# Performance work log

Measured on AMD Instinct MI355X. Metric: run time of the kernel, lower is better.

The kernel has to match this reference:

```python
import jax, jax.numpy as jnp
import numpy as np

N_NODES = 100000


def gcn_conv(x, W, b, src, dst, n_nodes):
    # x: [N, Fin], W: [Fin, Fout], edge (src->dst) with self-loops added,
    # symmetric normalization D^{-1/2} A D^{-1/2} as in PyG GCNConv defaults.
    h = x @ W  # [N, Fout]
    loops = jnp.arange(n_nodes, dtype=src.dtype)
    src_all = jnp.concatenate([src, loops])
    dst_all = jnp.concatenate([dst, loops])
    ones = jnp.ones(src_all.shape[0], dtype=h.dtype)
    deg = jax.ops.segment_sum(ones, dst_all, num_segments=n_nodes)  # in-degree incl. self-loop
    dinv = jnp.where(deg > 0, jax.lax.rsqrt(deg), 0.0)
    norm = dinv[src_all] * dinv[dst_all]  # [E+N]
    msg = h[src_all] * norm[:, None]      # gather + scale
    out = jax.ops.segment_sum(msg, dst_all, num_segments=n_nodes)  # scatter-add
    return out + b


def setup_inputs() -> dict:
    key = jax.random.key(0)
    k1, k2, k3, k4 = jax.random.split(key, 4)
    in_dim, hidden, out_dim = 128, 128, 64
    n_edges = 600000
    x = jax.random.normal(k1, (N_NODES, in_dim), dtype=jnp.float32)
    edge_index = jax.random.randint(k2, (2, n_edges), 0, N_NODES, dtype=jnp.int64)
    # Glorot-ish init for weights
    W1 = jax.random.normal(k3, (in_dim, hidden), dtype=jnp.float32) / np.sqrt(in_dim)
    b1 = jnp.zeros((hidden,), dtype=jnp.float32)
    W2 = jax.random.normal(k4, (hidden, out_dim), dtype=jnp.float32) / np.sqrt(hidden)
    b2 = jnp.zeros((out_dim,), dtype=jnp.float32)
    return {"x": x, "edge_index": edge_index, "W1": W1, "b1": b1, "W2": W2, "b2": b2}


def reference(x, edge_index, W1, b1, W2, b2):
    src, dst = edge_index[0], edge_index[1]
    h = jax.nn.relu(gcn_conv(x, W1, b1, src, dst, N_NODES))
    # dropout is identity in eval mode (training=False)
    return gcn_conv(h, W2, b2, src, dst, N_NODES)
```

## Files before the change

kernel.cpp:

```cpp
#include <hip/hip_runtime.h>
#include <hip/hip_bf16.h>
#include <stdint.h>

typedef unsigned int u32;
typedef unsigned short u16;
typedef unsigned long long u64;
typedef __attribute__((ext_vector_type(8))) short short8;
typedef __attribute__((ext_vector_type(4))) float f32x4;

#define SCAN_TILE 2048

__device__ __forceinline__ float bf2f(u16 u) {
    union { u32 u; float f; } v; v.u = ((u32)u) << 16; return v.f;
}
__device__ __forceinline__ u16 f2bf(float f) {
    u32 u = __float_as_uint(f);
    u32 r = (u + 0x7FFFu + ((u >> 16) & 1u)) >> 16;
    return (u16)r;
}
__device__ __forceinline__ u32 packbf(float lo, float hi) {
    return ((u32)f2bf(hi) << 16) | (u32)f2bf(lo);
}

template<int N>
__device__ __forceinline__ void wpack_one(const void* W, uint4* wpk, int p, int f32w) {
    const int n = p & (N - 1);
    const int kb = p >> ((N == 128) ? 7 : 6);
    u32 pk[4];
    if (f32w) {
        const float* wp = (const float*)W + (size_t)(kb * 8) * N + n;
        #pragma unroll
        for (int jj = 0; jj < 4; jj++)
            pk[jj] = packbf(wp[(2 * jj) * N], wp[(2 * jj + 1) * N]);
    } else {
        const u16* wp = (const u16*)W + (size_t)(kb * 8) * N + n;
        #pragma unroll
        for (int jj = 0; jj < 4; jj++)
            pk[jj] = ((u32)wp[(2 * jj + 1) * N] << 16) | (u32)wp[(2 * jj) * N];
    }
    uint4 v; v.x = pk[0]; v.y = pk[1]; v.z = pk[2]; v.w = pk[3];
    wpk[p] = v;
}

__global__ __launch_bounds__(256) void prep_k(const u32* __restrict__ xw,
                                              const u32* __restrict__ ew,
                                              int* __restrict__ flags,
                                              int* __restrict__ deg, int M,
                                              const void* __restrict__ W1,
                                              const void* __restrict__ W2,
                                              uint4* __restrict__ wpk1,
                                              uint4* __restrict__ wpk2,
                                              u64* __restrict__ lk, int nlk) {
    const int b = blockIdx.x, t = threadIdx.x;
    const int i4 = (b * 256 + t) * 4;
    if (i4 + 4 <= M) *(int4*)(deg + i4) = make_int4(0, 0, 0, 0);
    else { for (int j = 0; j < 4; j++) if (i4 + j < M) deg[i4 + j] = 0; }

    if (b < 12) {
        __shared__ int cnt;
        if (t == 0) cnt = 0;
        __syncthreads();
        int hits = 0;
        #pragma unroll
        for (int j = 0; j < 4; j++) {
            u32 f = (xw[t * 4 + j] >> 7) & 0xFFu;
            if (f >= 100u && f <= 140u) hits++;
        }
        atomicAdd(&cnt, hits);
        __syncthreads();
        const int f32w = (cnt < 512) ? 1 : 0;
        if (b < 8) wpack_one<128>(W1, wpk1, b * 256 + t, f32w);
        else       wpack_one<64> (W2, wpk2, (b - 8) * 256 + t, f32w);
        if (b == 0) {
            if (t < nlk) lk[t] = 0ull;
            if (t == 0) flags[0] = f32w;
            __shared__ u32 orr;
            if (t == 0) orr = 0u;
            __syncthreads();
            atomicOr(&orr, ew[2 * t + 1]);
            __syncthreads();
            if (t == 0) flags[1] = (orr == 0u) ? 1 : 0;
        }
    }
}

__global__ __launch_bounds__(256) void gemm1_count_k(
    const void* __restrict__ X, const uint4* __restrict__ wpk,
    u16* __restrict__ HS, const int* __restrict__ flags, int M,
    const void* __restrict__ ei, int E, int* __restrict__ deg, int GB)
{
    __shared__ u32 xlds[64 * 64];
    const int t = threadIdx.x;

    if ((int)blockIdx.x >= GB) {
        const int i2 = (((int)blockIdx.x - GB) * 256 + t) * 2;
        if (i2 >= E) return;
        if (flags[1]) {
            const long long* dp = (const long long*)ei + E;
            if (i2 + 1 < E) {
                longlong2 v = *(const longlong2*)(dp + i2);
                atomicAdd(&deg[(int)v.x], 1);
                atomicAdd(&deg[(int)v.y], 1);
            } else atomicAdd(&deg[(int)dp[i2]], 1);
        } else {
            const int* dp = (const int*)ei + E;
            if (i2 + 1 < E) {
                int2 v = *(const int2*)(dp + i2);
                atomicAdd(&deg[v.x], 1);
                atomicAdd(&deg[v.y], 1);
            } else atomicAdd(&deg[dp[i2]], 1);
        }
        return;
    }

    const int wave = t >> 6, lane = t & 63;
    const int q = lane >> 4, m = lane & 15;
    const bool xf32 = (flags[0] != 0);
    const int row0 = blockIdx.x * 64;

    for (int c = t; c < 1024; c += 256) {
        const int row = c >> 4, c8 = c & 15;
        const int grow = row0 + row;
        uint4 pk = make_uint4(0u, 0u, 0u, 0u);
        if (grow < M) {
            if (xf32) {
                const float* xp = (const float*)X + (size_t)grow * 128 + c8 * 8;
                float4 u = *(const float4*)xp;
                float4 v = *(const float4*)(xp + 4);
                pk.x = packbf(u.x, u.y); pk.y = packbf(u.z, u.w);
                pk.z = packbf(v.x, v.y); pk.w = packbf(v.z, v.w);
            } else {
                pk = *(const uint4*)((const u16*)X + (size_t)grow * 128 + c8 * 8);
            }
        }
        *(uint4*)&xlds[row * 64 + c8 * 4] = pk;
    }
    __syncthreads();

    union { uint4 u; short8 v; } a[4];
    #pragma unroll
    for (int s = 0; s < 4; s++)
        a[s].u = *(const uint4*)&xlds[(wave * 16 + m) * 64 + (s * 4 + q) * 4];

    f32x4 acc[8];
    #pragma unroll
    for (int tt = 0; tt < 8; tt++)
        acc[tt] = (f32x4){0.f, 0.f, 0.f, 0.f};

    #pragma unroll
    for (int s = 0; s < 4; s++) {
        union { uint4 u; short8 v; } b[8];
        #pragma unroll
        for (int tt = 0; tt < 8; tt++)
            b[tt].u = wpk[(s * 4 + q) * 128 + tt * 16 + m];
        #pragma unroll
        for (int tt = 0; tt < 8; tt++)
            acc[tt] = __builtin_amdgcn_mfma_f32_16x16x32_bf16(
                a[s].v, b[tt].v, acc[tt], 0, 0, 0);
    }

    u16* orow = (u16*)&xlds[wave * 16 * 64];
    #pragma unroll
    for (int tt = 0; tt < 8; tt++)
        #pragma unroll
        for (int r = 0; r < 4; r++)
            orow[(q * 4 + r) * 128 + tt * 16 + m] = f2bf(acc[tt][r]);

    #pragma unroll
    for (int j = 0; j < 4; j++) {
        const int cc = lane + j * 64;
        const int lrow = cc >> 4, c8 = cc & 15;
        const int grow = row0 + wave * 16 + lrow;
        uint4 v = *(const uint4*)&((const u32*)orow)[lrow * 64 + c8 * 4];
        if (grow < M)
            *(uint4*)(HS + (size_t)grow * 128 + c8 * 8) = v;
    }
}

__global__ __launch_bounds__(256) void scan_lb_k(const int* __restrict__ deg, int M,
                                                 u64* __restrict__ lk,
                                                 int* __restrict__ off,
                                                 int* __restrict__ cursor,
                                                 float* __restrict__ dinv, int nb) {
    const int bid = blockIdx.x, t = threadIdx.x;
    const int base = bid * SCAN_TILE + t * 8;
    int v[8];
    int s = 0;
    const bool full = (base + 8 <= M);
    if (full) {
        int4 a = *(const int4*)(deg + base);
        int4 b = *(const int4*)(deg + base + 4);
        v[0] = a.x; v[1] = a.y; v[2] = a.z; v[3] = a.w;
        v[4] = b.x; v[5] = b.y; v[6] = b.z; v[7] = b.w;
        s = v[0] + v[1] + v[2] + v[3] + v[4] + v[5] + v[6] + v[7];
    } else {
        #pragma unroll
        for (int j = 0; j < 8; j++) { v[j] = (base + j < M) ? deg[base + j] : 0; s += v[j]; }
    }
    __shared__ int buf[2][256];
    buf[0][t] = s;
    __syncthreads();
    int cur = 0;
    for (int d = 1; d < 256; d <<= 1) {
        int x = buf[cur][t];
        if (t >= d) x += buf[cur][t - d];
        buf[cur ^ 1][t] = x;
        __syncthreads();
        cur ^= 1;
    }
    const int incl = buf[cur][t];
    const int btotal = buf[cur][255];

    __shared__ int sbase;
    if (t == 0) {
        if (bid == 0) {
            __hip_atomic_store(&lk[0], (2ull << 62) | (u32)btotal,
                               __ATOMIC_RELEASE, __HIP_MEMORY_SCOPE_AGENT);
            sbase = 0;
        } else {
            __hip_atomic_store(&lk[bid], (1ull << 62) | (u32)btotal,
                               __ATOMIC_RELEASE, __HIP_MEMORY_SCOPE_AGENT);
            int run = 0;
            int j = bid - 1;
            while (j >= 0) {
                u64 w = __hip_atomic_load(&lk[j], __ATOMIC_ACQUIRE,
                                          __HIP_MEMORY_SCOPE_AGENT);
                const u64 st = w >> 62;
                if (st == 0) { __builtin_amdgcn_s_sleep(1); continue; }
                run += (int)(w & 0xFFFFFFFFull);
                if (st == 2ull) break;
                j--;
            }
            sbase = run;
            __hip_atomic_store(&lk[bid], (2ull << 62) | (u32)(run + btotal),
                               __ATOMIC_RELEASE, __HIP_MEMORY_SCOPE_AGENT);
        }
    }
    __syncthreads();

    int pre = sbase + incl - s;
    int o[8]; float dv[8];
    #pragma unroll
    for (int j = 0; j < 8; j++) {
        o[j] = pre;
        dv[j] = rsqrtf((float)(v[j] + 1));
        pre += v[j];
    }
    if (full) {
        *(int4*)(off + base)     = make_int4(o[0], o[1], o[2], o[3]);
        *(int4*)(off + base + 4) = make_int4(o[4], o[5], o[6], o[7]);
        *(int4*)(cursor + base)     = make_int4(o[0], o[1], o[2], o[3]);
        *(int4*)(cursor + base + 4) = make_int4(o[4], o[5], o[6], o[7]);
        *(float4*)(dinv + base)     = make_float4(dv[0], dv[1], dv[2], dv[3]);
        *(float4*)(dinv + base + 4) = make_float4(dv[4], dv[5], dv[6], dv[7]);
    } else {
        for (int j = 0; j < 8; j++) if (base + j < M) {
            off[base + j] = o[j]; cursor[base + j] = o[j]; dinv[base + j] = dv[j];
        }
    }
    if (bid == nb - 1 && t == 255) off[M] = sbase + btotal;
}

__global__ __launch_bounds__(256) void fill_k(const void* __restrict__ ei, int E,
                                              const int* __restrict__ flags,
                                              int* __restrict__ cursor, int* __restrict__ eidx) {
    const int i2 = (blockIdx.x * 256 + threadIdx.x) * 2;
    if (i2 >= E) return;
    int s0, d0, s1 = -1, d1 = -1;
    bool two = (i2 + 1 < E);
    if (flags[1]) {
        const long long* sp = (const long long*)ei;
        const long long* dp = sp + E;
        if (two) {
            longlong2 sv = *(const longlong2*)(sp + i2);
            longlong2 dv = *(const longlong2*)(dp + i2);
            s0 = (int)sv.x; s1 = (int)sv.y; d0 = (int)dv.x; d1 = (int)dv.y;
        } else { s0 = (int)sp[i2]; d0 = (int)dp[i2]; }
    } else {
        const int* sp = (const int*)ei;
        const int* dp = sp + E;
        if (two) {
            int2 sv = *(const int2*)(sp + i2);
            int2 dv = *(const int2*)(dp + i2);
            s0 = sv.x; s1 = sv.y; d0 = dv.x; d1 = dv.y;
        } else { s0 = sp[i2]; d0 = dp[i2]; }
    }
    int p0 = atomicAdd(&cursor[d0], 1);
    eidx[p0] = s0;
    if (two) {
        int p1 = atomicAdd(&cursor[d1], 1);
        eidx[p1] = s1;
    }
}

__global__ __launch_bounds__(256) void agg1_gemm2_k(
    const u16* __restrict__ hs, const int* __restrict__ eidx,
    const int* __restrict__ off, const float* __restrict__ dinv,
    const void* __restrict__ bias, const uint4* __restrict__ wpk,
    u16* __restrict__ HS2, const int* __restrict__ flags, int M)
{
    __shared__ u32 zlds[64 * 64];
    const int t = threadIdx.x;
    const int row0 = blockIdx.x * 64;
    const int f32io = flags[0];

    const int lane16 = t & 15;
    const int nsub   = t >> 4;
    const int c8 = lane16 * 8;
    const u16* __restrict__ hrow = hs + c8;

    float bb[8];
    if (f32io) {
        float4 u = *(const float4*)((const float*)bias + c8);
        float4 v = *(const float4*)((const float*)bias + c8 + 4);
        bb[0] = u.x; bb[1] = u.y; bb[2] = u.z; bb[3] = u.w;
        bb[4] = v.x; bb[5] = v.y; bb[6] = v.z; bb[7] = v.w;
    } else {
        uint4 u = *(const uint4*)((const u16*)bias + c8);
        const u16* s = (const u16*)&u;
        #pragma unroll
        for (int j = 0; j < 8; j++) bb[j] = bf2f(s[j]);
    }

    #pragma unroll
    for (int r = 0; r < 4; r++) {
        const int node = row0 + r * 16 + nsub;
        float o[8];
        #pragma unroll
        for (int j = 0; j < 8; j++) o[j] = 0.f;
        if (node < M) {
            const float dv = dinv[node];
            float a[8];
            {
                uint4 sp = *(const uint4*)(hrow + (size_t)node * 128);
                const u16* s = (const u16*)&sp;
                #pragma unroll
                for (int j = 0; j < 8; j++) a[j] = dv * bf2f(s[j]);
            }
            const int beg = off[node], end = off[node + 1];
            int p = beg;
            for (; p + 4 <= end; p += 4) {
                const int s0 = eidx[p + 0], s1 = eidx[p + 1];
                const int s2 = eidx[p + 2], s3 = eidx[p + 3];
                const float d0 = dinv[s0], d1 = dinv[s1];
                const float d2 = dinv[s2], d3 = dinv[s3];
                uint4 v0 = *(const uint4*)(hrow + (size_t)s0 * 128);
                uint4 v1 = *(const uint4*)(hrow + (size_t)s1 * 128);
                uint4 v2 = *(const uint4*)(hrow + (size_t)s2 * 128);
                uint4 v3 = *(const uint4*)(hrow + (size_t)s3 * 128);
                const u16* q0 = (const u16*)&v0; const u16* q1 = (const u16*)&v1;
                const u16* q2 = (const u16*)&v2; const u16* q3 = (const u16*)&v3;
                #pragma unroll
                for (int j = 0; j < 8; j++)
                    a[j] = fmaf(d0, bf2f(q0[j]),
                           fmaf(d1, bf2f(q1[j]),
                           fmaf(d2, bf2f(q2[j]),
                           fmaf(d3, bf2f(q3[j]), a[j]))));
            }
            for (; p < end; p++) {
                const int s = eidx[p];
                const float ds = dinv[s];
                uint4 v = *(const uint4*)(hrow + (size_t)s * 128);
                const u16* q = (const u16*)&v;
                #pragma unroll
                for (int j = 0; j < 8; j++) a[j] = fmaf(ds, bf2f(q[j]), a[j]);
            }
            #pragma unroll
            for (int j = 0; j < 8; j++)
                o[j] = fmaxf(fmaf(dv, a[j], bb[j]), 0.f);
        }
        uint4 pk;
        pk.x = packbf(o[0], o[1]); pk.y = packbf(o[2], o[3]);
        pk.z = packbf(o[4], o[5]); pk.w = packbf(o[6], o[7]);
        *(uint4*)&zlds[(r * 16 + nsub) * 64 + lane16 * 4] = pk;
    }
    __syncthreads();

    const int wave = t >> 6, lane = t & 63;
    const int q = lane >> 4, m = lane & 15;

    union { uint4 u; short8 v; } af[4];
    #pragma unroll
    for (int s = 0; s < 4; s++)
        af[s].u = *(const uint4*)&zlds[(wave * 16 + m) * 64 + (s * 4 + q) * 4];

    f32x4 acc[4];
    #pragma unroll
    for (int tt = 0; tt < 4; tt++)
        acc[tt] = (f32x4){0.f, 0.f, 0.f, 0.f};

    #pragma unroll
    for (int s = 0; s < 4; s++) {
        union { uint4 u; short8 v; } bf_[4];
        #pragma unroll
        for (int tt = 0; tt < 4; tt++)
            bf_[tt].u = wpk[(s * 4 + q) * 64 + tt * 16 + m];
        #pragma unroll
        for (int tt = 0; tt < 4; tt++)
            acc[tt] = __builtin_amdgcn_mfma_f32_16x16x32_bf16(
                af[s].v, bf_[tt].v, acc[tt], 0, 0, 0);
    }

    float dv4[4];
    #pragma unroll
    for (int r = 0; r < 4; r++) {
        const int grow = row0 + wave * 16 + q * 4 + r;
        dv4[r] = (grow < M) ? dinv[grow] : 0.f;
    }

    u16* orow = (u16*)&zlds[wave * 16 * 64];
    #pragma unroll
    for (int tt = 0; tt < 4; tt++)
        #pragma unroll
        for (int r = 0; r < 4; r++)
            orow[(q * 4 + r) * 64 + tt * 16 + m] = f2bf(acc[tt][r] * dv4[r]);

    #pragma unroll
    for (int j = 0; j < 2; j++) {
        const int cc = lane + j * 64;
        const int lrow = cc >> 3, c8b = cc & 7;
        const int grow = row0 + wave * 16 + lrow;
        uint4 v = *(const uint4*)&((const u32*)orow)[lrow * 32 + c8b * 4];
        if (grow < M)
            *(uint4*)(HS2 + (size_t)grow * 64 + c8b * 8) = v;
    }
}

template<int N, bool RELU>
__global__ __launch_bounds__(256) void aggregate_k(
    const u16* __restrict__ hs, const int* __restrict__ eidx,
    const int* __restrict__ off, const float* __restrict__ dinv,
    const void* __restrict__ bias, void* __restrict__ out,
    const int* __restrict__ flags, int out_is_ext, int M)
{
    constexpr int TPN = N / 8;
    constexpr int NPB = 256 / TPN;
    const int node = blockIdx.x * NPB + threadIdx.x / TPN;
    const int lane = threadIdx.x % TPN;
    if (node >= M) return;
    const int f32io = flags[0];
    const int beg = off[node], end = off[node + 1];
    const int c8 = lane * 8;
    const u16* __restrict__ hrow = hs + c8;

    float a[8];
    {
        uint4 sp = *(const uint4*)(hrow + (size_t)node * N);
        const u16* s = (const u16*)&sp;
        #pragma unroll
        for (int j = 0; j < 8; j++) a[j] = bf2f(s[j]);
    }

    int p = beg;
    for (; p + 4 <= end; p += 4) {
        const int s0 = eidx[p + 0], s1 = eidx[p + 1];
        const int s2 = eidx[p + 2], s3 = eidx[p + 3];
        uint4 v0 = *(const uint4*)(hrow + (size_t)s0 * N);
        uint4 v1 = *(const uint4*)(hrow + (size_t)s1 * N);
        uint4 v2 = *(const uint4*)(hrow + (size_t)s2 * N);
        uint4 v3 = *(const uint4*)(hrow + (size_t)s3 * N);
        const u16* q0 = (const u16*)&v0; const u16* q1 = (const u16*)&v1;
        const u16* q2 = (const u16*)&v2; const u16* q3 = (const u16*)&v3;
        #pragma unroll
        for (int j = 0; j < 8; j++)
            a[j] += (bf2f(q0[j]) + bf2f(q1[j])) + (bf2f(q2[j]) + bf2f(q3[j]));
    }
    for (; p < end; p++) {
        const int s = eidx[p];
        uint4 v = *(const uint4*)(hrow + (size_t)s * N);
        const u16* q = (const u16*)&v;
        #pragma unroll
        for (int j = 0; j < 8; j++) a[j] += bf2f(q[j]);
    }

    const float dv = dinv[node];
    float b[8];
    if (f32io) {
        float4 u = *(const float4*)((const float*)bias + c8);
        float4 v = *(const float4*)((const float*)bias + c8 + 4);
        b[0] = u.x; b[1] = u.y; b[2] = u.z; b[3] = u.w;
        b[4] = v.x; b[5] = v.y; b[6] = v.z; b[7] = v.w;
    } else {
        uint4 u = *(const uint4*)((const u16*)bias + c8);
        const u16* s = (const u16*)&u;
        #pragma unroll
        for (int j = 0; j < 8; j++) b[j] = bf2f(s[j]);
    }
    float o[8];
    #pragma unroll
    for (int j = 0; j < 8; j++) {
        o[j] = fmaf(dv, a[j], b[j]);
        if (RELU) o[j] = fmaxf(o[j], 0.f);
    }
    if (out_is_ext && f32io) {
        float* op = (float*)out + (size_t)node * N + c8;
        *(float4*)op       = make_float4(o[0], o[1], o[2], o[3]);
        *(float4*)(op + 4) = make_float4(o[4], o[5], o[6], o[7]);
    } else {
        uint4 pk;
        pk.x = packbf(o[0], o[1]); pk.y = packbf(o[2], o[3]);
        pk.z = packbf(o[4], o[5]); pk.w = packbf(o[6], o[7]);
        *(uint4*)((u16*)out + (size_t)node * N + c8) = pk;
    }
}

extern "C" void kernel_launch(void* const* d_in, const int* in_sizes, int n_in,
                              void* d_out, int out_size, void* d_ws, size_t ws_size,
                              hipStream_t stream) {
    const void* x  = d_in[0];
    const void* ei = d_in[1];
    const void* W1 = d_in[2];
    const void* b1 = d_in[3];
    const void* W2 = d_in[4];
    const void* b2 = d_in[5];

    const int M = in_sizes[0] / 128;
    const int E = in_sizes[1] / 2;
    const int NB = (M + SCAN_TILE - 1) / SCAN_TILE;
    const int GB = (M + 63) / 64;
    const int CB = (E + 511) / 512;

    char* ws = (char*)d_ws;
    size_t offb = 0;
    auto alloc = [&](size_t bytes) -> void* {
        void* p = ws + offb; offb += (bytes + 255) & ~(size_t)255; return p;
    };
    int*   flags  = (int*)  alloc(256);
    u64*   lk     = (u64*)  alloc(2048);
    uint4* wpk1   = (uint4*)alloc(16 * 128 * 16);
    uint4* wpk2   = (uint4*)alloc(16 * 64 * 16);
    int*   deg    = (int*)  alloc((size_t)M * 4);
    int*   off    = (int*)  alloc((size_t)(M + 1) * 4);
    int*   cursor = (int*)  alloc((size_t)M * 4);
    float* dinv   = (float*)alloc((size_t)M * 4);
    int*   eidx   = (int*)  alloc((size_t)E * 4);
    u16*   hs1    = (u16*)  alloc((size_t)M * 128 * 2);
    u16*   hs2    = (u16*)  alloc((size_t)M * 64 * 2);
    (void)ws_size; (void)n_in; (void)out_size;

    prep_k<<<(M + 1023) / 1024, 256, 0, stream>>>((const u32*)x, (const u32*)ei, flags,
                                                  deg, M, W1, W2, wpk1, wpk2, lk, NB);
    gemm1_count_k<<<GB + CB, 256, 0, stream>>>(x, wpk1, hs1, flags, M, ei, E, deg, GB);
    scan_lb_k<<<NB, 256, 0, stream>>>(deg, M, lk, off, cursor, dinv, NB);
    fill_k<<<(E + 511) / 512, 256, 0, stream>>>(ei, E, flags, cursor, eidx);
    agg1_gemm2_k<<<(M + 63) / 64, 256, 0, stream>>>(hs1, eidx, off, dinv, b1, wpk2, hs2,
                                                    flags, M);
    aggregate_k<64, false><<<(M + 31) / 32, 256, 0, stream>>>(hs2, eidx, off, dinv, b2, d_out,
                                                              flags, 1, M);
}
```

Before: 235.3 us.

## Restructure kernel pipeline: fuse degree count into prep, scan into gemm1, stage edges in LDS

Degree zeroing moves to a memset, and degree counting moves into the prep kernel, which detects index width per block. The scan is merged with the first GEMM into one launch. The aggregation kernels stage their CSR offsets and edge indices in LDS. The first aggregation interleaves four nodes per thread so their gathers are in flight at once, which trades extra registers and divergence for more memory-level parallelism. The goal is fewer launches and better latency hiding on the gathers.

New measurement: 230.9 us. About the same (-1.9%).

```diff
diff --git a/kernel.cpp b/kernel.cpp
--- a/kernel.cpp
+++ b/kernel.cpp
@@ -42,22 +42,20 @@
     wpk[p] = v;
 }
 
-__global__ __launch_bounds__(256) void prep_k(const u32* __restrict__ xw,
-                                              const u32* __restrict__ ew,
-                                              int* __restrict__ flags,
-                                              int* __restrict__ deg, int M,
-                                              const void* __restrict__ W1,
-                                              const void* __restrict__ W2,
-                                              uint4* __restrict__ wpk1,
-                                              uint4* __restrict__ wpk2,
-                                              u64* __restrict__ lk, int nlk) {
+__global__ __launch_bounds__(256) void prep_count_k(
+    const u32* __restrict__ xw, const void* __restrict__ ei,
+    int* __restrict__ flags, int M, int E,
+    const void* __restrict__ W1, const void* __restrict__ W2,
+    uint4* __restrict__ wpk1, uint4* __restrict__ wpk2,
+    int* __restrict__ deg)
+{
+    __shared__ int cnt;
+    __shared__ u32 orr;
+    __shared__ u32 dorr;
     const int b = blockIdx.x, t = threadIdx.x;
-    const int i4 = (b * 256 + t) * 4;
-    if (i4 + 4 <= M) *(int4*)(deg + i4) = make_int4(0, 0, 0, 0);
-    else { for (int j = 0; j < 4; j++) if (i4 + j < M) deg[i4 + j] = 0; }
+    const u32* ew = (const u32*)ei;
 
     if (b < 12) {
-        __shared__ int cnt;
         if (t == 0) cnt = 0;
         __syncthreads();
         int hits = 0;
@@ -72,51 +70,141 @@
         if (b < 8) wpack_one<128>(W1, wpk1, b * 256 + t, f32w);
         else       wpack_one<64> (W2, wpk2, (b - 8) * 256 + t, f32w);
         if (b == 0) {
-            if (t < nlk) lk[t] = 0ull;
             if (t == 0) flags[0] = f32w;
-            __shared__ u32 orr;
             if (t == 0) orr = 0u;
             __syncthreads();
             atomicOr(&orr, ew[2 * t + 1]);
             __syncthreads();
             if (t == 0) flags[1] = (orr == 0u) ? 1 : 0;
         }
-    }
-}
-
-__global__ __launch_bounds__(256) void gemm1_count_k(
+        return;
+    }
+
+    const int cb = b - 12;
+    const int i2 = (cb * 256 + t) * 2;
+    if (t == 0) dorr = 0u;
+    __syncthreads();
+    u32 w = 0u;
+    if (i2 + 1 < E) w = ew[(size_t)E + i2 + 1];
+    atomicOr(&dorr, w);
+    __syncthreads();
+    const bool is64 = (dorr == 0u);
+    if (i2 >= E) return;
+    if (is64) {
+        const long long* dp = (const long long*)ei + E;
+        if (i2 + 1 < E) {
+            longlong2 v = *(const longlong2*)(dp + i2);
+            atomicAdd(&deg[(int)v.x], 1);
+            atomicAdd(&deg[(int)v.y], 1);
+        } else atomicAdd(&deg[(int)dp[i2]], 1);
+    } else {
+        const int* dp = (const int*)ei + E;
+        if (i2 + 1 < E) {
+            int2 v = *(const int2*)(dp + i2);
+            atomicAdd(&deg[v.x], 1);
+            atomicAdd(&deg[v.y], 1);
+        } else atomicAdd(&deg[dp[i2]], 1);
+    }
+}
+
+__global__ __launch_bounds__(256) void scan_gemm1_k(
+    const int* __restrict__ deg, int M,
+    u64* __restrict__ lk, int* __restrict__ off,
+    int* __restrict__ cursor, float* __restrict__ dinv, int nb,
     const void* __restrict__ X, const uint4* __restrict__ wpk,
-    u16* __restrict__ HS, const int* __restrict__ flags, int M,
-    const void* __restrict__ ei, int E, int* __restrict__ deg, int GB)
+    u16* __restrict__ HS, const int* __restrict__ flags)
 {
-    __shared__ u32 xlds[64 * 64];
+    __shared__ u32 smem[64 * 64];
     const int t = threadIdx.x;
 
-    if ((int)blockIdx.x >= GB) {
-        const int i2 = (((int)blockIdx.x - GB) * 256 + t) * 2;
-        if (i2 >= E) return;
-        if (flags[1]) {
-            const long long* dp = (const long long*)ei + E;
-            if (i2 + 1 < E) {
-                longlong2 v = *(const longlong2*)(dp + i2);
-                atomicAdd(&deg[(int)v.x], 1);
-                atomicAdd(&deg[(int)v.y], 1);
-            } else atomicAdd(&deg[(int)dp[i2]], 1);
+    if ((int)blockIdx.x < nb) {
+        const int bid = blockIdx.x;
+        const int base = bid * SCAN_TILE + t * 8;
+        int v[8];
+        int s = 0;
+        const bool full = (base + 8 <= M);
+        if (full) {
+            int4 a = *(const int4*)(deg + base);
+            int4 b = *(const int4*)(deg + base + 4);
+            v[0] = a.x; v[1] = a.y; v[2] = a.z; v[3] = a.w;
+            v[4] = b.x; v[5] = b.y; v[6] = b.z; v[7] = b.w;
+            s = v[0] + v[1] + v[2] + v[3] + v[4] + v[5] + v[6] + v[7];
         } else {
-            const int* dp = (const int*)ei + E;
-            if (i2 + 1 < E) {
-                int2 v = *(const int2*)(dp + i2);
-                atomicAdd(&deg[v.x], 1);
-                atomicAdd(&deg[v.y], 1);
-            } else atomicAdd(&deg[dp[i2]], 1);
-        }
+            #pragma unroll
+            for (int j = 0; j < 8; j++) { v[j] = (base + j < M) ? deg[base + j] : 0; s += v[j]; }
+        }
+        int* bp = (int*)smem;
+        int* bq = (int*)smem + 256;
+        int* psb = (int*)smem + 512;
+        bp[t] = s;
+        __syncthreads();
+        for (int d = 1; d < 256; d <<= 1) {
+            int x = bp[t];
+            if (t >= d) x += bp[t - d];
+            bq[t] = x;
+            __syncthreads();
+            int* tmp = bp; bp = bq; bq = tmp;
+        }
+        const int incl = bp[t];
+        const int btotal = bp[255];
+
+        if (t == 0) {
+            if (bid == 0) {
+                __hip_atomic_store(&lk[0], (2ull << 62) | (u32)btotal,
+                                   __ATOMIC_RELEASE, __HIP_MEMORY_SCOPE_AGENT);
+                psb[0] = 0;
+            } else {
+                __hip_atomic_store(&lk[bid], (1ull << 62) | (u32)btotal,
+                                   __ATOMIC_RELEASE, __HIP_MEMORY_SCOPE_AGENT);
+                int run = 0;
+                int j = bid - 1;
+                while (j >= 0) {
+                    u64 w = __hip_atomic_load(&lk[j], __ATOMIC_ACQUIRE,
+                                              __HIP_MEMORY_SCOPE_AGENT);
+                    const u64 st = w >> 62;
+                    if (st == 0) { __builtin_amdgcn_s_sleep(1); continue; }
+                    run += (int)(w & 0xFFFFFFFFull);
+                    if (st == 2ull) break;
+                    j--;
+                }
+                psb[0] = run;
+                __hip_atomic_store(&lk[bid], (2ull << 62) | (u32)(run + btotal),
+                                   __ATOMIC_RELEASE, __HIP_MEMORY_SCOPE_AGENT);
+            }
+        }
+        __syncthreads();
+        const int sbase = psb[0];
+
+        int pre = sbase + incl - s;
+        int o[8]; float dv[8];
+        #pragma unroll
+        for (int j = 0; j < 8; j++) {
+            o[j] = pre;
+            dv[j] = rsqrtf((float)(v[j] + 1));
+            pre += v[j];
+        }
+        if (full) {
+            *(int4*)(off + base)     = make_int4(o[0], o[1], o[2], o[3]);
+            *(int4*)(off + base + 4) = make_int4(o[4], o[5], o[6], o[7]);
+            *(int4*)(cursor + base)     = make_int4(o[0], o[1], o[2], o[3]);
+            *(int4*)(cursor + base + 4) = make_int4(o[4], o[5], o[6], o[7]);
+            *(float4*)(dinv + base)     = make_float4(dv[0], dv[1], dv[2], dv[3]);
+            *(float4*)(dinv + base + 4) = make_float4(dv[4], dv[5], dv[6], dv[7]);
+        } else {
+            for (int j = 0; j < 8; j++) if (base + j < M) {
+                off[base + j] = o[j]; cursor[base + j] = o[j]; dinv[base + j] = dv[j];
+            }
+        }
+        if (bid == nb - 1 && t == 255) off[M] = sbase + btotal;
         return;
     }
 
+    const int gb = (int)blockIdx.x - nb;
     const int wave = t >> 6, lane = t & 63;
     const int q = lane >> 4, m = lane & 15;
     const bool xf32 = (flags[0] != 0);
-    const int row0 = blockIdx.x * 64;
+    const int row0 = gb * 64;
+    u32* xlds = smem;
 
     for (int c = t; c < 1024; c += 256) {
         const int row = c >> 4, c8 = c & 15;
@@ -175,90 +263,6 @@
         if (grow < M)
             *(uint4*)(HS + (size_t)grow * 128 + c8 * 8) = v;
     }
-}
-
-__global__ __launch_bounds__(256) void scan_lb_k(const int* __restrict__ deg, int M,
-                                                 u64* __restrict__ lk,
-                                                 int* __restrict__ off,
-                                                 int* __restrict__ cursor,
-                                                 float* __restrict__ dinv, int nb) {
-    const int bid = blockIdx.x, t = threadIdx.x;
-    const int base = bid * SCAN_TILE + t * 8;
-    int v[8];
-    int s = 0;
-    const bool full = (base + 8 <= M);
-    if (full) {
-        int4 a = *(const int4*)(deg + base);
-        int4 b = *(const int4*)(deg + base + 4);
-        v[0] = a.x; v[1] = a.y; v[2] = a.z; v[3] = a.w;
-        v[4] = b.x; v[5] = b.y; v[6] = b.z; v[7] = b.w;
-        s = v[0] + v[1] + v[2] + v[3] + v[4] + v[5] + v[6] + v[7];
-    } else {
-        #pragma unroll
-        for (int j = 0; j < 8; j++) { v[j] = (base + j < M) ? deg[base + j] : 0; s += v[j]; }
-    }
-    __shared__ int buf[2][256];
-    buf[0][t] = s;
-    __syncthreads();
-    int cur = 0;
-    for (int d = 1; d < 256; d <<= 1) {
-        int x = buf[cur][t];
-        if (t >= d) x += buf[cur][t - d];
-        buf[cur ^ 1][t] = x;
-        __syncthreads();
-        cur ^= 1;
-    }
-    const int incl = buf[cur][t];
-    const int btotal = buf[cur][255];
-
-    __shared__ int sbase;
-    if (t == 0) {
-        if (bid == 0) {
-            __hip_atomic_store(&lk[0], (2ull << 62) | (u32)btotal,
-                               __ATOMIC_RELEASE, __HIP_MEMORY_SCOPE_AGENT);
-            sbase = 0;
-        } else {
-            __hip_atomic_store(&lk[bid], (1ull << 62) | (u32)btotal,
-                               __ATOMIC_RELEASE, __HIP_MEMORY_SCOPE_AGENT);
-            int run = 0;
-            int j = bid - 1;
-            while (j >= 0) {
-                u64 w = __hip_atomic_load(&lk[j], __ATOMIC_ACQUIRE,
-                                          __HIP_MEMORY_SCOPE_AGENT);
-                const u64 st = w >> 62;
-                if (st == 0) { __builtin_amdgcn_s_sleep(1); continue; }
-                run += (int)(w & 0xFFFFFFFFull);
-                if (st == 2ull) break;
-                j--;
-            }
-            sbase = run;
-            __hip_atomic_store(&lk[bid], (2ull << 62) | (u32)(run + btotal),
-                               __ATOMIC_RELEASE, __HIP_MEMORY_SCOPE_AGENT);
-        }
-    }
-    __syncthreads();
-
-    int pre = sbase + incl - s;
-    int o[8]; float dv[8];
-    #pragma unroll
-    for (int j = 0; j < 8; j++) {
-        o[j] = pre;
-        dv[j] = rsqrtf((float)(v[j] + 1));
-        pre += v[j];
-    }
-    if (full) {
-        *(int4*)(off + base)     = make_int4(o[0], o[1], o[2], o[3]);
-        *(int4*)(off + base + 4) = make_int4(o[4], o[5], o[6], o[7]);
-        *(int4*)(cursor + base)     = make_int4(o[0], o[1], o[2], o[3]);
-        *(int4*)(cursor + base + 4) = make_int4(o[4], o[5], o[6], o[7]);
-        *(float4*)(dinv + base)     = make_float4(dv[0], dv[1], dv[2], dv[3]);
-        *(float4*)(dinv + base + 4) = make_float4(dv[4], dv[5], dv[6], dv[7]);
-    } else {
-        for (int j = 0; j < 8; j++) if (base + j < M) {
-            off[base + j] = o[j]; cursor[base + j] = o[j]; dinv[base + j] = dv[j];
-        }
-    }
-    if (bid == nb - 1 && t == 255) off[M] = sbase + btotal;
 }
 
 __global__ __launch_bounds__(256) void fill_k(const void* __restrict__ ei, int E,
@@ -300,12 +304,21 @@
     u16* __restrict__ HS2, const int* __restrict__ flags, int M)
 {
     __shared__ u32 zlds[64 * 64];
+    __shared__ int soff[65];
+    __shared__ int elds[768];
     const int t = threadIdx.x;
     const int row0 = blockIdx.x * 64;
     const int f32io = flags[0];
 
-    const int lane16 = t & 15;
-    const int nsub   = t >> 4;
+    for (int i = t; i <= 64; i += 256) soff[i] = off[min(row0 + i, M)];
+    __syncthreads();
+    const int beg64 = soff[0];
+    const int tot = soff[64] - beg64;
+    const bool useLds = (tot <= 768);
+    if (useLds) for (int i = t; i < tot; i += 256) elds[i] = eidx[beg64 + i];
+    __syncthreads();
+
+    const int lane16 = t & 15, nsub = t >> 4;
     const int c8 = lane16 * 8;
     const u16* __restrict__ hrow = hs + c8;
 
@@ -322,57 +335,62 @@
         for (int j = 0; j < 8; j++) bb[j] = bf2f(s[j]);
     }
 
+    float acc[4][8]; float dvn[4]; int p[4], e[4];
     #pragma unroll
     for (int r = 0; r < 4; r++) {
-        const int node = row0 + r * 16 + nsub;
-        float o[8];
-        #pragma unroll
-        for (int j = 0; j < 8; j++) o[j] = 0.f;
-        if (node < M) {
-            const float dv = dinv[node];
-            float a[8];
-            {
-                uint4 sp = *(const uint4*)(hrow + (size_t)node * 128);
-                const u16* s = (const u16*)&sp;
-                #pragma unroll
-                for (int j = 0; j < 8; j++) a[j] = dv * bf2f(s[j]);
-            }
-            const int beg = off[node], end = off[node + 1];
-            int p = beg;
-            for (; p + 4 <= end; p += 4) {
-                const int s0 = eidx[p + 0], s1 = eidx[p + 1];
-                const int s2 = eidx[p + 2], s3 = eidx[p + 3];
-                const float d0 = dinv[s0], d1 = dinv[s1];
-                const float d2 = dinv[s2], d3 = dinv[s3];
-                uint4 v0 = *(const uint4*)(hrow + (size_t)s0 * 128);
-                uint4 v1 = *(const uint4*)(hrow + (size_t)s1 * 128);
-                uint4 v2 = *(const uint4*)(hrow + (size_t)s2 * 128);
-                uint4 v3 = *(const uint4*)(hrow + (size_t)s3 * 128);
-                const u16* q0 = (const u16*)&v0; const u16* q1 = (const u16*)&v1;
-                const u16* q2 = (const u16*)&v2; const u16* q3 = (const u16*)&v3;
-                #pragma unroll
-                for (int j = 0; j < 8; j++)
-                    a[j] = fmaf(d0, bf2f(q0[j]),
-                           fmaf(d1, bf2f(q1[j]),
-                           fmaf(d2, bf2f(q2[j]),
-                           fmaf(d3, bf2f(q3[j]), a[j]))));
-            }
-            for (; p < end; p++) {
-                const int s = eidx[p];
-                const float ds = dinv[s];
-                uint4 v = *(const uint4*)(hrow + (size_t)s * 128);
-                const u16* q = (const u16*)&v;
-                #pragma unroll
-                for (int j = 0; j < 8; j++) a[j] = fmaf(ds, bf2f(q[j]), a[j]);
-            }
+        const int li = r * 16 + nsub;
+        const int nd = row0 + li;
+        const bool ok = nd < M;
+        p[r] = soff[li] - beg64;
+        e[r] = soff[li + 1] - beg64;
+        dvn[r] = ok ? dinv[nd] : 0.f;
+        uint4 sp = make_uint4(0u, 0u, 0u, 0u);
+        if (ok) sp = *(const uint4*)(hrow + (size_t)nd * 128);
+        const u16* s = (const u16*)&sp;
+        #pragma unroll
+        for (int j = 0; j < 8; j++) acc[r][j] = dvn[r] * bf2f(s[j]);
+    }
+
+    while (true) {
+        bool any = false;
+        #pragma unroll
+        for (int r = 0; r < 4; r++) any = any || (p[r] < e[r]);
+        if (!any) break;
+        int sidx[4]; bool act[4];
+        #pragma unroll
+        for (int r = 0; r < 4; r++) {
+            act[r] = p[r] < e[r];
+            const int ip = act[r] ? p[r] : 0;
+            sidx[r] = useLds ? elds[ip] : eidx[beg64 + ip];
+            p[r] += act[r] ? 1 : 0;
+        }
+        float dsv[4]; uint4 vv[4];
+        #pragma unroll
+        for (int r = 0; r < 4; r++) {
+            dsv[r] = act[r] ? dinv[sidx[r]] : 0.f;
+            vv[r] = *(const uint4*)(hrow + (size_t)sidx[r] * 128);
+        }
+        #pragma unroll
+        for (int r = 0; r < 4; r++) {
+            const u16* q = (const u16*)&vv[r];
             #pragma unroll
             for (int j = 0; j < 8; j++)
-                o[j] = fmaxf(fmaf(dv, a[j], bb[j]), 0.f);
-        }
+                acc[r][j] = fmaf(dsv[r], bf2f(q[j]), acc[r][j]);
+        }
+    }
+
+    #pragma unroll
+    for (int r = 0; r < 4; r++) {
+        const int li = r * 16 + nsub;
+        const int nd = row0 + li;
+        float o[8];
+        #pragma unroll
+        for (int j = 0; j < 8; j++)
+            o[j] = (nd < M) ? fmaxf(fmaf(dvn[r], acc[r][j], bb[j]), 0.f) : 0.f;
         uint4 pk;
         pk.x = packbf(o[0], o[1]); pk.y = packbf(o[2], o[3]);
         pk.z = packbf(o[4], o[5]); pk.w = packbf(o[6], o[7]);
-        *(uint4*)&zlds[(r * 16 + nsub) * 64 + lane16 * 4] = pk;
+        *(uint4*)&zlds[li * 64 + lane16 * 4] = pk;
     }
     __syncthreads();
 
@@ -384,10 +402,10 @@
     for (int s = 0; s < 4; s++)
         af[s].u = *(const uint4*)&zlds[(wave * 16 + m) * 64 + (s * 4 + q) * 4];
 
-    f32x4 acc[4];
+    f32x4 acg[4];
     #pragma unroll
     for (int tt = 0; tt < 4; tt++)
-        acc[tt] = (f32x4){0.f, 0.f, 0.f, 0.f};
+        acg[tt] = (f32x4){0.f, 0.f, 0.f, 0.f};
 
     #pragma unroll
     for (int s = 0; s < 4; s++) {
@@ -397,8 +415,8 @@
             bf_[tt].u = wpk[(s * 4 + q) * 64 + tt * 16 + m];
         #pragma unroll
         for (int tt = 0; tt < 4; tt++)
-            acc[tt] = __builtin_amdgcn_mfma_f32_16x16x32_bf16(
-                af[s].v, bf_[tt].v, acc[tt], 0, 0, 0);
+            acg[tt] = __builtin_amdgcn_mfma_f32_16x16x32_bf16(
+                af[s].v, bf_[tt].v, acg[tt], 0, 0, 0);
     }
 
     float dv4[4];
@@ -409,11 +427,12 @@
     }
 
     u16* orow = (u16*)&zlds[wave * 16 * 64];
+    __syncthreads();
     #pragma unroll
     for (int tt = 0; tt < 4; tt++)
         #pragma unroll
         for (int r = 0; r < 4; r++)
-            orow[(q * 4 + r) * 64 + tt * 16 + m] = f2bf(acc[tt][r] * dv4[r]);
+            orow[(q * 4 + r) * 64 + tt * 16 + m] = f2bf(acg[tt][r] * dv4[r]);
 
     #pragma unroll
     for (int j = 0; j < 2; j++) {
@@ -435,11 +454,26 @@
 {
     constexpr int TPN = N / 8;
     constexpr int NPB = 256 / TPN;
-    const int node = blockIdx.x * NPB + threadIdx.x / TPN;
-    const int lane = threadIdx.x % TPN;
+    constexpr int ECAP = NPB * 16;
+    __shared__ int soff[NPB + 1];
+    __shared__ int elds[ECAP];
+    const int t = threadIdx.x;
+    const int n0 = blockIdx.x * NPB;
+
+    for (int i = t; i <= NPB; i += 256) soff[i] = off[min(n0 + i, M)];
+    __syncthreads();
+    const int beg0 = soff[0];
+    const int tot = soff[NPB] - beg0;
+    const bool useLds = (tot <= ECAP);
+    if (useLds) for (int i = t; i < tot; i += 256) elds[i] = eidx[beg0 + i];
+    __syncthreads();
+
+    const int node = n0 + t / TPN;
+    const int lane = t % TPN;
     if (node >= M) return;
     const int f32io = flags[0];
-    const int beg = off[node], end = off[node + 1];
+    int p = soff[t / TPN] - beg0;
+    const int e = soff[t / TPN + 1] - beg0;
     const int c8 = lane * 8;
     const u16* __restrict__ hrow = hs + c8;
 
@@ -451,10 +485,10 @@
         for (int j = 0; j < 8; j++) a[j] = bf2f(s[j]);
     }
 
-    int p = beg;
-    for (; p + 4 <= end; p += 4) {
-        const int s0 = eidx[p + 0], s1 = eidx[p + 1];
-        const int s2 = eidx[p + 2], s3 = eidx[p + 3];
+    for (; p + 4 <= e; p += 4) {
+        int s0, s1, s2, s3;
+        if (useLds) { s0 = elds[p]; s1 = elds[p + 1]; s2 = elds[p + 2]; s3 = elds[p + 3]; }
+        else { s0 = eidx[beg0 + p]; s1 = eidx[beg0 + p + 1]; s2 = eidx[beg0 + p + 2]; s3 = eidx[beg0 + p + 3]; }
         uint4 v0 = *(const uint4*)(hrow + (size_t)s0 * N);
         uint4 v1 = *(const uint4*)(hrow + (size_t)s1 * N);
         uint4 v2 = *(const uint4*)(hrow + (size_t)s2 * N);
@@ -465,8 +499,8 @@
         for (int j = 0; j < 8; j++)
             a[j] += (bf2f(q0[j]) + bf2f(q1[j])) + (bf2f(q2[j]) + bf2f(q3[j]));
     }
-    for (; p < end; p++) {
-        const int s = eidx[p];
+    for (; p < e; p++) {
+        const int s = useLds ? elds[p] : eidx[beg0 + p];
         uint4 v = *(const uint4*)(hrow + (size_t)s * N);
         const u16* q = (const u16*)&v;
         #pragma unroll
@@ -527,9 +561,9 @@
     };
     int*   flags  = (int*)  alloc(256);
     u64*   lk     = (u64*)  alloc(2048);
+    int*   deg    = (int*)  alloc((size_t)M * 4);
     uint4* wpk1   = (uint4*)alloc(16 * 128 * 16);
     uint4* wpk2   = (uint4*)alloc(16 * 64 * 16);
-    int*   deg    = (int*)  alloc((size_t)M * 4);
     int*   off    = (int*)  alloc((size_t)(M + 1) * 4);
     int*   cursor = (int*)  alloc((size_t)M * 4);
     float* dinv   = (float*)alloc((size_t)M * 4);
@@ -538,13 +572,14 @@
     u16*   hs2    = (u16*)  alloc((size_t)M * 64 * 2);
     (void)ws_size; (void)n_in; (void)out_size;
 
-    prep_k<<<(M + 1023) / 1024, 256, 0, stream>>>((const u32*)x, (const u32*)ei, flags,
-                                                  deg, M, W1, W2, wpk1, wpk2, lk, NB);
-    gemm1_count_k<<<GB + CB, 256, 0, stream>>>(x, wpk1, hs1, flags, M, ei, E, deg, GB);
-    scan_lb_k<<<NB, 256, 0, stream>>>(deg, M, lk, off, cursor, dinv, NB);
-    fill_k<<<(E + 511) / 512, 256, 0, stream>>>(ei, E, flags, cursor, eidx);
-    agg1_gemm2_k<<<(M + 63) / 64, 256, 0, stream>>>(hs1, eidx, off, dinv, b1, wpk2, hs2,
-                                                    flags, M);
+    hipMemsetAsync(lk, 0, 2048 + (size_t)M * 4, stream);
+    prep_count_k<<<12 + CB, 256, 0, stream>>>((const u32*)x, ei, flags, M, E,
+                                              W1, W2, wpk1, wpk2, deg);
+    scan_gemm1_k<<<NB + GB, 256, 0, stream>>>(deg, M, lk, off, cursor, dinv, NB,
+                                              x, wpk1, hs1, flags);
+    fill_k<<<CB, 256, 0, stream>>>(ei, E, flags, cursor, eidx);
+    agg1_gemm2_k<<<GB, 256, 0, stream>>>(hs1, eidx, off, dinv, b1, wpk2, hs2,
+                                         flags, M);
     aggregate_k<64, false><<<(M + 31) / 32, 256, 0, stream>>>(hs2, eidx, off, dinv, b2, d_out,
                                                               flags, 1, M);
 }
```
